# Kernel optimization log

Measured on AMD Instinct MI355X. Metric: run time of the kernel, lower is better.

Reference implementation:

```python
import jax, jax.numpy as jnp
import numpy as np

B, D, H = 524288, 128, 64  # batch, input_dim, hidden_dim; mask_dim = transform_dim = D//2 = 64


def _mlp(x, Wh, bh, Wo, bo):
    """eqx.nn.MLP with depth=3: 3 hidden relu layers then linear out.
    x: [B, in]; Wh: [3, H, in/H]; bh: [3, H]; Wo: [out, H]; bo: [out]."""
    h = x
    for i in range(Wh.shape[0]):  # fixed small layer loop
        h = jax.nn.relu(h @ Wh[i].T + bh[i])
    return h @ Wo.T + bo


def setup_inputs() -> dict:
    key = jax.random.key(0)
    ks = jax.random.split(key, 9)
    m = D // 2
    s = 1.0 / np.sqrt(H)  # lecun-ish init scale
    inp = {"x": jax.random.normal(ks[0], (B, D), dtype=jnp.float32)}
    inp["cond_Wh"] = jax.random.normal(ks[1], (3, H, m), dtype=jnp.float32) * s
    inp["cond_bh"] = jnp.zeros((3, H), dtype=jnp.float32)
    inp["cond_Wo"] = jax.random.normal(ks[2], (D - m, H), dtype=jnp.float32) * s
    inp["cond_bo"] = jnp.zeros((D - m,), dtype=jnp.float32)
    inp["scale_Wh"] = jax.random.normal(ks[3], (3, H, m), dtype=jnp.float32) * s
    inp["scale_bh"] = jnp.zeros((3, H), dtype=jnp.float32)
    inp["scale_Wo"] = jax.random.normal(ks[4], (D - m, H), dtype=jnp.float32) * s
    inp["scale_bo"] = jnp.zeros((D - m,), dtype=jnp.float32)
    return inp


def reference(x, cond_Wh, cond_bh, cond_Wo, cond_bo,
              scale_Wh, scale_bh, scale_Wo, scale_bo):
    m = x.shape[-1] // 2
    # mask = [1]*m + [0]*(D-m) -> mask_idx = [:m], transform_idx = [m:] (static contiguous split)
    x_masked = x[..., :m]
    x_transform = x[..., m:]
    shift = _mlp(x_masked, cond_Wh, cond_bh, cond_Wo, cond_bo)        # [B, D-m]
    log_scale = _mlp(x_masked, scale_Wh, scale_bh, scale_Wo, scale_bo)  # [B, D-m]
    scale = jnp.exp(jnp.clip(log_scale, -5, 3))
    y_transform = x_transform * scale + shift
    y = jnp.concatenate([x_masked, y_transform], axis=-1)  # scatter back (contiguous)
    logdet = jnp.sum(log_scale, axis=-1)  # note: unclipped log_scale, as in original
    return y, logdet
```

## Files before the change

### kernel.cpp

```cpp
#include <hip/hip_runtime.h>
#include <hip/hip_bf16.h>
#include <cstdint>

typedef __attribute__((ext_vector_type(8))) short short8;
typedef __attribute__((ext_vector_type(4))) float f32x4;
typedef __attribute__((ext_vector_type(4))) unsigned int u32x4;

__device__ __forceinline__ uint32_t pk_bf16(float a, float b) {
    uint32_t ua = (uint32_t)__builtin_bit_cast(unsigned short, __float2bfloat16(a));
    uint32_t ub = (uint32_t)__builtin_bit_cast(unsigned short, __float2bfloat16(b));
    return ua | (ub << 16);
}
__device__ __forceinline__ void split_pair(float a, float b, uint32_t& H, uint32_t& L) {
    H = pk_bf16(a, b);
    float fa = __uint_as_float(H << 16);
    float fb = __uint_as_float(H & 0xffff0000u);
    L = pk_bf16(a - fa, b - fb);
}
__device__ __forceinline__ short8 mk8(uint32_t a, uint32_t b, uint32_t c, uint32_t d) {
    u32x4 v; v[0] = a; v[1] = b; v[2] = c; v[3] = d;
    return __builtin_bit_cast(short8, v);
}
__device__ __forceinline__ void cvt_frag(f32x4 A, f32x4 Bv, short8& hi, short8& lo) {
    uint32_t h0, l0, h1, l1, h2, l2, h3, l3;
    split_pair(A[0],  A[1],  h0, l0);
    split_pair(A[2],  A[3],  h1, l1);
    split_pair(Bv[0], Bv[1], h2, l2);
    split_pair(Bv[2], Bv[3], h3, l3);
    hi = mk8(h0, h1, h2, h3);
    lo = mk8(l0, l1, l2, l3);
}

__global__ void prep_weights(const float* __restrict__ cWh, const float* __restrict__ cWo,
                             const float* __restrict__ sWh, const float* __restrict__ sWo,
                             unsigned short* __restrict__ wf) {
    int t = blockIdx.x * 256 + threadIdx.x;
    int e    = t & 7;
    int mt   = (t >> 3) & 3;
    int lane = (t >> 5) & 63;
    int kp   = (t >> 11) & 1;
    int L    = (t >> 12) & 7;
    const float* src = (L < 3)  ? cWh + L * 4096
                     : (L == 3) ? cWo
                     : (L < 7)  ? sWh + (L - 4) * 4096
                     :            sWo;
    int m = mt * 16 + (lane & 15);
    int k = (2 * kp + (e >> 2)) * 16 + 4 * (lane >> 4) + (e & 3);
    float w = src[m * 64 + k];
    uint32_t H, Lo;
    split_pair(w, w, H, Lo);
    int off = lane * 32 + mt * 8 + e;
    int fi = (L * 2 + kp) * 2;
    wf[fi * 2048 + off]        = (unsigned short)H;
    wf[(fi + 1) * 2048 + off]  = (unsigned short)Lo;
}

__device__ __forceinline__ void run_layer(const unsigned short* __restrict__ wf, int Lid,
                                          const float* __restrict__ bias, int lane, int g4,
                                          const short8 Bh[2][4], const short8 Bl[2][4],
                                          f32x4 acc[4][4]) {
#pragma unroll
    for (int mt = 0; mt < 4; ++mt) {
        f32x4 bb = *(const f32x4*)(bias + mt * 16 + g4);
#pragma unroll
        for (int nt = 0; nt < 4; ++nt) acc[mt][nt] = bb;
    }
#pragma unroll
    for (int kp = 0; kp < 2; ++kp) {
        short8 Ah[4], Al[4];
        const unsigned short* p = wf + (Lid * 2 + kp) * 4096 + lane * 32;
#pragma unroll
        for (int mt = 0; mt < 4; ++mt) {
            Ah[mt] = *(const short8*)(p + mt * 8);
            Al[mt] = *(const short8*)(p + 2048 + mt * 8);
        }
#pragma unroll
        for (int nt = 0; nt < 4; ++nt)
#pragma unroll
            for (int mt = 0; mt < 4; ++mt) {
                acc[mt][nt] = __builtin_amdgcn_mfma_f32_16x16x32_bf16(Ah[mt], Bh[kp][nt], acc[mt][nt], 0, 0, 0);
                acc[mt][nt] = __builtin_amdgcn_mfma_f32_16x16x32_bf16(Al[mt], Bh[kp][nt], acc[mt][nt], 0, 0, 0);
                acc[mt][nt] = __builtin_amdgcn_mfma_f32_16x16x32_bf16(Ah[mt], Bl[kp][nt], acc[mt][nt], 0, 0, 0);
            }
    }
}

template<bool RELU>
__device__ __forceinline__ void acc_to_B(const f32x4 acc[4][4], short8 Bh[2][4], short8 Bl[2][4]) {
#pragma unroll
    for (int kp = 0; kp < 2; ++kp)
#pragma unroll
        for (int nt = 0; nt < 4; ++nt) {
            f32x4 a = acc[2 * kp][nt], b = acc[2 * kp + 1][nt];
            if (RELU) {
#pragma unroll
                for (int i = 0; i < 4; ++i) { a[i] = fmaxf(a[i], 0.f); b[i] = fmaxf(b[i], 0.f); }
            }
            cvt_frag(a, b, Bh[kp][nt], Bl[kp][nt]);
        }
}

__global__ __launch_bounds__(64, 2)
void coupling_main(const float* __restrict__ x,
                   const float* __restrict__ cbh, const float* __restrict__ cbo,
                   const float* __restrict__ sbh, const float* __restrict__ sbo,
                   const unsigned short* __restrict__ wf,
                   float* __restrict__ y, float* __restrict__ logdet) {
    const int lane = threadIdx.x;
    const int c = lane & 15;
    const int g4 = (lane >> 4) * 4;
    const long row0 = (long)blockIdx.x * 64;
    const float* xr = x + (row0 + c) * 128 + g4;
    float* yr = y + (row0 + c) * 128 + g4;

    f32x4 xm[4][4];
#pragma unroll
    for (int nt = 0; nt < 4; ++nt)
#pragma unroll
        for (int kt = 0; kt < 4; ++kt)
            xm[nt][kt] = *(const f32x4*)(xr + nt * 2048 + kt * 16);
#pragma unroll
    for (int nt = 0; nt < 4; ++nt)
#pragma unroll
        for (int kt = 0; kt < 4; ++kt)
            *(f32x4*)(yr + nt * 2048 + kt * 16) = xm[nt][kt];

    short8 B0h[2][4], B0l[2][4];
#pragma unroll
    for (int kp = 0; kp < 2; ++kp)
#pragma unroll
        for (int nt = 0; nt < 4; ++nt)
            cvt_frag(xm[nt][2 * kp], xm[nt][2 * kp + 1], B0h[kp][nt], B0l[kp][nt]);

    f32x4 acc[4][4];
    short8 Bh[2][4], Bl[2][4];

    run_layer(wf, 0, cbh,       lane, g4, B0h, B0l, acc);
    acc_to_B<true>(acc, Bh, Bl);
    run_layer(wf, 1, cbh + 64,  lane, g4, Bh, Bl, acc);
    acc_to_B<true>(acc, Bh, Bl);
    run_layer(wf, 2, cbh + 128, lane, g4, Bh, Bl, acc);
    acc_to_B<true>(acc, Bh, Bl);
    run_layer(wf, 3, cbo,       lane, g4, Bh, Bl, acc);
    f32x4 shift[4][4];
#pragma unroll
    for (int mt = 0; mt < 4; ++mt)
#pragma unroll
        for (int nt = 0; nt < 4; ++nt) shift[mt][nt] = acc[mt][nt];

    run_layer(wf, 4, sbh,       lane, g4, B0h, B0l, acc);
    acc_to_B<true>(acc, Bh, Bl);
    run_layer(wf, 5, sbh + 64,  lane, g4, Bh, Bl, acc);
    acc_to_B<true>(acc, Bh, Bl);
    run_layer(wf, 6, sbh + 128, lane, g4, Bh, Bl, acc);
    acc_to_B<true>(acc, Bh, Bl);
    run_layer(wf, 7, sbo,       lane, g4, Bh, Bl, acc);

    f32x4 xt[4][4];
#pragma unroll
    for (int nt = 0; nt < 4; ++nt)
#pragma unroll
        for (int mt = 0; mt < 4; ++mt)
            xt[nt][mt] = *(const f32x4*)(xr + nt * 2048 + 64 + mt * 16);

    float pld0 = 0.f, pld1 = 0.f, pld2 = 0.f, pld3 = 0.f;
#pragma unroll
    for (int nt = 0; nt < 4; ++nt) {
        float psum = 0.f;
#pragma unroll
        for (int mt = 0; mt < 4; ++mt) {
            f32x4 ls = acc[mt][nt];
            psum += ls[0] + ls[1] + ls[2] + ls[3];
            f32x4 o;
#pragma unroll
            for (int i = 0; i < 4; ++i) {
                float cl = fminf(fmaxf(ls[i], -5.f), 3.f);
                o[i] = xt[nt][mt][i] * __expf(cl) + shift[mt][nt][i];
            }
            *(f32x4*)(yr + nt * 2048 + 64 + mt * 16) = o;
        }
        if (nt == 0) pld0 = psum; else if (nt == 1) pld1 = psum;
        else if (nt == 2) pld2 = psum; else pld3 = psum;
    }
#pragma unroll
    for (int nt = 0; nt < 4; ++nt) {
        float v = (nt == 0) ? pld0 : (nt == 1) ? pld1 : (nt == 2) ? pld2 : pld3;
        v += __shfl_xor(v, 16);
        v += __shfl_xor(v, 32);
        if ((lane >> 4) == 0) logdet[row0 + nt * 16 + c] = v;
    }
}

extern "C" void kernel_launch(void* const* d_in, const int* in_sizes, int n_in,
                              void* d_out, int out_size, void* d_ws, size_t ws_size,
                              hipStream_t stream) {
    const float* x   = (const float*)d_in[0];
    const float* cWh = (const float*)d_in[1];
    const float* cbh = (const float*)d_in[2];
    const float* cWo = (const float*)d_in[3];
    const float* cbo = (const float*)d_in[4];
    const float* sWh = (const float*)d_in[5];
    const float* sbh = (const float*)d_in[6];
    const float* sWo = (const float*)d_in[7];
    const float* sbo = (const float*)d_in[8];

    const int B = in_sizes[0] / 128;

    unsigned short* wf = (unsigned short*)d_ws;

    prep_weights<<<128, 256, 0, stream>>>(cWh, cWo, sWh, sWo, wf);

    float* y = (float*)d_out;
    float* logdet = y + (size_t)B * 128;
    coupling_main<<<B / 64, 64, 0, stream>>>(x, cbh, cbo, sbh, sbo, wf, y, logdet);
}
```

Measured before the change: 174.3 us.

## Halve per-wave row tile, pack shift as bf16, use nontemporal stores

```diff
diff --git a/kernel.cpp b/kernel.cpp
--- a/kernel.cpp
+++ b/kernel.cpp
@@ -21,6 +21,9 @@
     u32x4 v; v[0] = a; v[1] = b; v[2] = c; v[3] = d;
     return __builtin_bit_cast(short8, v);
 }
+__device__ __forceinline__ float bf16lo(uint32_t p) { return __uint_as_float(p << 16); }
+__device__ __forceinline__ float bf16hi(uint32_t p) { return __uint_as_float(p & 0xffff0000u); }
+
 __device__ __forceinline__ void cvt_frag(f32x4 A, f32x4 Bv, short8& hi, short8& lo) {
     uint32_t h0, l0, h1, l1, h2, l2, h3, l3;
     split_pair(A[0],  A[1],  h0, l0);
@@ -57,13 +60,13 @@
 
 __device__ __forceinline__ void run_layer(const unsigned short* __restrict__ wf, int Lid,
                                           const float* __restrict__ bias, int lane, int g4,
-                                          const short8 Bh[2][4], const short8 Bl[2][4],
-                                          f32x4 acc[4][4]) {
+                                          const short8 Bh[2][2], const short8 Bl[2][2],
+                                          f32x4 acc[4][2]) {
 #pragma unroll
     for (int mt = 0; mt < 4; ++mt) {
         f32x4 bb = *(const f32x4*)(bias + mt * 16 + g4);
 #pragma unroll
-        for (int nt = 0; nt < 4; ++nt) acc[mt][nt] = bb;
+        for (int nt = 0; nt < 2; ++nt) acc[mt][nt] = bb;
     }
 #pragma unroll
     for (int kp = 0; kp < 2; ++kp) {
@@ -75,7 +78,7 @@
             Al[mt] = *(const short8*)(p + 2048 + mt * 8);
         }
 #pragma unroll
-        for (int nt = 0; nt < 4; ++nt)
+        for (int nt = 0; nt < 2; ++nt)
 #pragma unroll
             for (int mt = 0; mt < 4; ++mt) {
                 acc[mt][nt] = __builtin_amdgcn_mfma_f32_16x16x32_bf16(Ah[mt], Bh[kp][nt], acc[mt][nt], 0, 0, 0);
@@ -85,106 +88,102 @@
     }
 }
 
-template<bool RELU>
-__device__ __forceinline__ void acc_to_B(const f32x4 acc[4][4], short8 Bh[2][4], short8 Bl[2][4]) {
+__device__ __forceinline__ void acc_to_B_relu(const f32x4 acc[4][2], short8 Bh[2][2], short8 Bl[2][2]) {
 #pragma unroll
     for (int kp = 0; kp < 2; ++kp)
 #pragma unroll
-        for (int nt = 0; nt < 4; ++nt) {
+        for (int nt = 0; nt < 2; ++nt) {
             f32x4 a = acc[2 * kp][nt], b = acc[2 * kp + 1][nt];
-            if (RELU) {
-#pragma unroll
-                for (int i = 0; i < 4; ++i) { a[i] = fmaxf(a[i], 0.f); b[i] = fmaxf(b[i], 0.f); }
-            }
+#pragma unroll
+            for (int i = 0; i < 4; ++i) { a[i] = fmaxf(a[i], 0.f); b[i] = fmaxf(b[i], 0.f); }
             cvt_frag(a, b, Bh[kp][nt], Bl[kp][nt]);
         }
 }
 
-__global__ __launch_bounds__(64, 2)
+__global__ __launch_bounds__(256, 3)
 void coupling_main(const float* __restrict__ x,
                    const float* __restrict__ cbh, const float* __restrict__ cbo,
                    const float* __restrict__ sbh, const float* __restrict__ sbo,
                    const unsigned short* __restrict__ wf,
                    float* __restrict__ y, float* __restrict__ logdet) {
-    const int lane = threadIdx.x;
+    const int lane = threadIdx.x & 63;
+    const int wid = threadIdx.x >> 6;
     const int c = lane & 15;
     const int g4 = (lane >> 4) * 4;
-    const long row0 = (long)blockIdx.x * 64;
+    const long row0 = (long)blockIdx.x * 128 + wid * 32;
     const float* xr = x + (row0 + c) * 128 + g4;
     float* yr = y + (row0 + c) * 128 + g4;
 
-    f32x4 xm[4][4];
-#pragma unroll
-    for (int nt = 0; nt < 4; ++nt)
+    f32x4 xm[2][4];
+#pragma unroll
+    for (int nt = 0; nt < 2; ++nt)
 #pragma unroll
         for (int kt = 0; kt < 4; ++kt)
             xm[nt][kt] = *(const f32x4*)(xr + nt * 2048 + kt * 16);
 #pragma unroll
-    for (int nt = 0; nt < 4; ++nt)
+    for (int nt = 0; nt < 2; ++nt)
 #pragma unroll
         for (int kt = 0; kt < 4; ++kt)
-            *(f32x4*)(yr + nt * 2048 + kt * 16) = xm[nt][kt];
-
-    short8 B0h[2][4], B0l[2][4];
+            __builtin_nontemporal_store(xm[nt][kt], (f32x4*)(yr + nt * 2048 + kt * 16));
+
+    short8 B0h[2][2], B0l[2][2];
 #pragma unroll
     for (int kp = 0; kp < 2; ++kp)
 #pragma unroll
-        for (int nt = 0; nt < 4; ++nt)
+        for (int nt = 0; nt < 2; ++nt)
             cvt_frag(xm[nt][2 * kp], xm[nt][2 * kp + 1], B0h[kp][nt], B0l[kp][nt]);
 
-    f32x4 acc[4][4];
-    short8 Bh[2][4], Bl[2][4];
+    f32x4 acc[4][2];
+    short8 Bh[2][2], Bl[2][2];
 
     run_layer(wf, 0, cbh,       lane, g4, B0h, B0l, acc);
-    acc_to_B<true>(acc, Bh, Bl);
+    acc_to_B_relu(acc, Bh, Bl);
     run_layer(wf, 1, cbh + 64,  lane, g4, Bh, Bl, acc);
-    acc_to_B<true>(acc, Bh, Bl);
+    acc_to_B_relu(acc, Bh, Bl);
     run_layer(wf, 2, cbh + 128, lane, g4, Bh, Bl, acc);
-    acc_to_B<true>(acc, Bh, Bl);
+    acc_to_B_relu(acc, Bh, Bl);
     run_layer(wf, 3, cbo,       lane, g4, Bh, Bl, acc);
-    f32x4 shift[4][4];
+    uint2 shiftp[4][2];
 #pragma unroll
     for (int mt = 0; mt < 4; ++mt)
 #pragma unroll
-        for (int nt = 0; nt < 4; ++nt) shift[mt][nt] = acc[mt][nt];
+        for (int nt = 0; nt < 2; ++nt) {
+            f32x4 v = acc[mt][nt];
+            shiftp[mt][nt].x = pk_bf16(v[0], v[1]);
+            shiftp[mt][nt].y = pk_bf16(v[2], v[3]);
+        }
 
     run_layer(wf, 4, sbh,       lane, g4, B0h, B0l, acc);
-    acc_to_B<true>(acc, Bh, Bl);
+    acc_to_B_relu(acc, Bh, Bl);
     run_layer(wf, 5, sbh + 64,  lane, g4, Bh, Bl, acc);
-    acc_to_B<true>(acc, Bh, Bl);
+    acc_to_B_relu(acc, Bh, Bl);
     run_layer(wf, 6, sbh + 128, lane, g4, Bh, Bl, acc);
-    acc_to_B<true>(acc, Bh, Bl);
+    acc_to_B_relu(acc, Bh, Bl);
     run_layer(wf, 7, sbo,       lane, g4, Bh, Bl, acc);
 
-    f32x4 xt[4][4];
-#pragma unroll
-    for (int nt = 0; nt < 4; ++nt)
-#pragma unroll
-        for (int mt = 0; mt < 4; ++mt)
-            xt[nt][mt] = *(const f32x4*)(xr + nt * 2048 + 64 + mt * 16);
-
-    float pld0 = 0.f, pld1 = 0.f, pld2 = 0.f, pld3 = 0.f;
-#pragma unroll
-    for (int nt = 0; nt < 4; ++nt) {
+    float pld0 = 0.f, pld1 = 0.f;
+#pragma unroll
+    for (int nt = 0; nt < 2; ++nt) {
         float psum = 0.f;
 #pragma unroll
         for (int mt = 0; mt < 4; ++mt) {
             f32x4 ls = acc[mt][nt];
             psum += ls[0] + ls[1] + ls[2] + ls[3];
+            f32x4 xt = *(const f32x4*)(xr + nt * 2048 + 64 + mt * 16);
             f32x4 o;
-#pragma unroll
-            for (int i = 0; i < 4; ++i) {
-                float cl = fminf(fmaxf(ls[i], -5.f), 3.f);
-                o[i] = xt[nt][mt][i] * __expf(cl) + shift[mt][nt][i];
-            }
-            *(f32x4*)(yr + nt * 2048 + 64 + mt * 16) = o;
-        }
-        if (nt == 0) pld0 = psum; else if (nt == 1) pld1 = psum;
-        else if (nt == 2) pld2 = psum; else pld3 = psum;
-    }
-#pragma unroll
-    for (int nt = 0; nt < 4; ++nt) {
-        float v = (nt == 0) ? pld0 : (nt == 1) ? pld1 : (nt == 2) ? pld2 : pld3;
+            float s0 = bf16lo(shiftp[mt][nt].x), s1 = bf16hi(shiftp[mt][nt].x);
+            float s2 = bf16lo(shiftp[mt][nt].y), s3 = bf16hi(shiftp[mt][nt].y);
+            o[0] = xt[0] * __expf(fminf(fmaxf(ls[0], -5.f), 3.f)) + s0;
+            o[1] = xt[1] * __expf(fminf(fmaxf(ls[1], -5.f), 3.f)) + s1;
+            o[2] = xt[2] * __expf(fminf(fmaxf(ls[2], -5.f), 3.f)) + s2;
+            o[3] = xt[3] * __expf(fminf(fmaxf(ls[3], -5.f), 3.f)) + s3;
+            __builtin_nontemporal_store(o, (f32x4*)(yr + nt * 2048 + 64 + mt * 16));
+        }
+        if (nt == 0) pld0 = psum; else pld1 = psum;
+    }
+#pragma unroll
+    for (int nt = 0; nt < 2; ++nt) {
+        float v = (nt == 0) ? pld0 : pld1;
         v += __shfl_xor(v, 16);
         v += __shfl_xor(v, 32);
         if ((lane >> 4) == 0) logdet[row0 + nt * 16 + c] = v;
@@ -212,5 +211,5 @@
 
     float* y = (float*)d_out;
     float* logdet = y + (size_t)B * 128;
-    coupling_main<<<B / 64, 64, 0, stream>>>(x, cbh, cbo, sbh, sbo, wf, y, logdet);
-}
+    coupling_main<<<B / 128, 256, 0, stream>>>(x, cbh, cbo, sbh, sbo, wf, y, logdet);
+}
```

Result: slower. 212.5 us (+21.9%).

## Switch split-bf16 MFMA to fp16 with split weights only, shrinking register state

Applied to the files above, without the earlier changes.

```diff
diff --git a/kernel.cpp b/kernel.cpp
--- a/kernel.cpp
+++ b/kernel.cpp
@@ -1,39 +1,13 @@
 #include <hip/hip_runtime.h>
-#include <hip/hip_bf16.h>
 #include <cstdint>
 
-typedef __attribute__((ext_vector_type(8))) short short8;
+typedef __attribute__((ext_vector_type(8))) _Float16 half8;
+typedef __attribute__((ext_vector_type(4))) _Float16 half4;
 typedef __attribute__((ext_vector_type(4))) float f32x4;
-typedef __attribute__((ext_vector_type(4))) unsigned int u32x4;
-
-__device__ __forceinline__ uint32_t pk_bf16(float a, float b) {
-    uint32_t ua = (uint32_t)__builtin_bit_cast(unsigned short, __float2bfloat16(a));
-    uint32_t ub = (uint32_t)__builtin_bit_cast(unsigned short, __float2bfloat16(b));
-    return ua | (ub << 16);
-}
-__device__ __forceinline__ void split_pair(float a, float b, uint32_t& H, uint32_t& L) {
-    H = pk_bf16(a, b);
-    float fa = __uint_as_float(H << 16);
-    float fb = __uint_as_float(H & 0xffff0000u);
-    L = pk_bf16(a - fa, b - fb);
-}
-__device__ __forceinline__ short8 mk8(uint32_t a, uint32_t b, uint32_t c, uint32_t d) {
-    u32x4 v; v[0] = a; v[1] = b; v[2] = c; v[3] = d;
-    return __builtin_bit_cast(short8, v);
-}
-__device__ __forceinline__ void cvt_frag(f32x4 A, f32x4 Bv, short8& hi, short8& lo) {
-    uint32_t h0, l0, h1, l1, h2, l2, h3, l3;
-    split_pair(A[0],  A[1],  h0, l0);
-    split_pair(A[2],  A[3],  h1, l1);
-    split_pair(Bv[0], Bv[1], h2, l2);
-    split_pair(Bv[2], Bv[3], h3, l3);
-    hi = mk8(h0, h1, h2, h3);
-    lo = mk8(l0, l1, l2, l3);
-}
 
 __global__ void prep_weights(const float* __restrict__ cWh, const float* __restrict__ cWo,
                              const float* __restrict__ sWh, const float* __restrict__ sWo,
-                             unsigned short* __restrict__ wf) {
+                             _Float16* __restrict__ wf) {
     int t = blockIdx.x * 256 + threadIdx.x;
     int e    = t & 7;
     int mt   = (t >> 3) & 3;
@@ -47,18 +21,30 @@
     int m = mt * 16 + (lane & 15);
     int k = (2 * kp + (e >> 2)) * 16 + 4 * (lane >> 4) + (e & 3);
     float w = src[m * 64 + k];
-    uint32_t H, Lo;
-    split_pair(w, w, H, Lo);
+    _Float16 hi = (_Float16)w;
+    _Float16 lo = (_Float16)(w - (float)hi);
     int off = lane * 32 + mt * 8 + e;
     int fi = (L * 2 + kp) * 2;
-    wf[fi * 2048 + off]        = (unsigned short)H;
-    wf[(fi + 1) * 2048 + off]  = (unsigned short)Lo;
+    wf[fi * 2048 + off]       = hi;
+    wf[(fi + 1) * 2048 + off] = lo;
 }
 
-__device__ __forceinline__ void run_layer(const unsigned short* __restrict__ wf, int Lid,
+template<bool RELU>
+__device__ __forceinline__ half8 cvt_frag(f32x4 a, f32x4 b) {
+    half8 r;
+#pragma unroll
+    for (int i = 0; i < 4; ++i) {
+        float va = RELU ? fmaxf(a[i], 0.f) : a[i];
+        float vb = RELU ? fmaxf(b[i], 0.f) : b[i];
+        r[i]     = (_Float16)va;
+        r[i + 4] = (_Float16)vb;
+    }
+    return r;
+}
+
+__device__ __forceinline__ void run_layer(const _Float16* __restrict__ wf, int Lid,
                                           const float* __restrict__ bias, int lane, int g4,
-                                          const short8 Bh[2][4], const short8 Bl[2][4],
-                                          f32x4 acc[4][4]) {
+                                          const half8 B[2][4], f32x4 acc[4][4]) {
 #pragma unroll
     for (int mt = 0; mt < 4; ++mt) {
         f32x4 bb = *(const f32x4*)(bias + mt * 16 + g4);
@@ -67,44 +53,36 @@
     }
 #pragma unroll
     for (int kp = 0; kp < 2; ++kp) {
-        short8 Ah[4], Al[4];
-        const unsigned short* p = wf + (Lid * 2 + kp) * 4096 + lane * 32;
+        half8 Ah[4], Al[4];
+        const _Float16* p = wf + (Lid * 2 + kp) * 4096 + lane * 32;
 #pragma unroll
         for (int mt = 0; mt < 4; ++mt) {
-            Ah[mt] = *(const short8*)(p + mt * 8);
-            Al[mt] = *(const short8*)(p + 2048 + mt * 8);
+            Ah[mt] = *(const half8*)(p + mt * 8);
+            Al[mt] = *(const half8*)(p + 2048 + mt * 8);
         }
 #pragma unroll
         for (int nt = 0; nt < 4; ++nt)
 #pragma unroll
             for (int mt = 0; mt < 4; ++mt) {
-                acc[mt][nt] = __builtin_amdgcn_mfma_f32_16x16x32_bf16(Ah[mt], Bh[kp][nt], acc[mt][nt], 0, 0, 0);
-                acc[mt][nt] = __builtin_amdgcn_mfma_f32_16x16x32_bf16(Al[mt], Bh[kp][nt], acc[mt][nt], 0, 0, 0);
-                acc[mt][nt] = __builtin_amdgcn_mfma_f32_16x16x32_bf16(Ah[mt], Bl[kp][nt], acc[mt][nt], 0, 0, 0);
+                acc[mt][nt] = __builtin_amdgcn_mfma_f32_16x16x32_f16(Ah[mt], B[kp][nt], acc[mt][nt], 0, 0, 0);
+                acc[mt][nt] = __builtin_amdgcn_mfma_f32_16x16x32_f16(Al[mt], B[kp][nt], acc[mt][nt], 0, 0, 0);
             }
     }
 }
 
-template<bool RELU>
-__device__ __forceinline__ void acc_to_B(const f32x4 acc[4][4], short8 Bh[2][4], short8 Bl[2][4]) {
+__device__ __forceinline__ void acc_to_B_relu(const f32x4 acc[4][4], half8 B[2][4]) {
 #pragma unroll
     for (int kp = 0; kp < 2; ++kp)
 #pragma unroll
-        for (int nt = 0; nt < 4; ++nt) {
-            f32x4 a = acc[2 * kp][nt], b = acc[2 * kp + 1][nt];
-            if (RELU) {
-#pragma unroll
-                for (int i = 0; i < 4; ++i) { a[i] = fmaxf(a[i], 0.f); b[i] = fmaxf(b[i], 0.f); }
-            }
-            cvt_frag(a, b, Bh[kp][nt], Bl[kp][nt]);
-        }
+        for (int nt = 0; nt < 4; ++nt)
+            B[kp][nt] = cvt_frag<true>(acc[2 * kp][nt], acc[2 * kp + 1][nt]);
 }
 
 __global__ __launch_bounds__(64, 2)
 void coupling_main(const float* __restrict__ x,
                    const float* __restrict__ cbh, const float* __restrict__ cbo,
                    const float* __restrict__ sbh, const float* __restrict__ sbo,
-                   const unsigned short* __restrict__ wf,
+                   const _Float16* __restrict__ wf,
                    float* __restrict__ y, float* __restrict__ logdet) {
     const int lane = threadIdx.x;
     const int c = lane & 15;
@@ -113,55 +91,49 @@
     const float* xr = x + (row0 + c) * 128 + g4;
     float* yr = y + (row0 + c) * 128 + g4;
 
-    f32x4 xm[4][4];
+    half8 B0[2][4];
 #pragma unroll
-    for (int nt = 0; nt < 4; ++nt)
-#pragma unroll
-        for (int kt = 0; kt < 4; ++kt)
-            xm[nt][kt] = *(const f32x4*)(xr + nt * 2048 + kt * 16);
-#pragma unroll
-    for (int nt = 0; nt < 4; ++nt)
-#pragma unroll
-        for (int kt = 0; kt < 4; ++kt)
-            *(f32x4*)(yr + nt * 2048 + kt * 16) = xm[nt][kt];
-
-    short8 B0h[2][4], B0l[2][4];
-#pragma unroll
-    for (int kp = 0; kp < 2; ++kp)
-#pragma unroll
-        for (int nt = 0; nt < 4; ++nt)
-            cvt_frag(xm[nt][2 * kp], xm[nt][2 * kp + 1], B0h[kp][nt], B0l[kp][nt]);
+    for (int nt = 0; nt < 4; ++nt) {
+        f32x4 v0 = *(const f32x4*)(xr + nt * 2048);
+        f32x4 v1 = *(const f32x4*)(xr + nt * 2048 + 16);
+        f32x4 v2 = *(const f32x4*)(xr + nt * 2048 + 32);
+        f32x4 v3 = *(const f32x4*)(xr + nt * 2048 + 48);
+        __builtin_nontemporal_store(v0, (f32x4*)(yr + nt * 2048));
+        __builtin_nontemporal_store(v1, (f32x4*)(yr + nt * 2048 + 16));
+        __builtin_nontemporal_store(v2, (f32x4*)(yr + nt * 2048 + 32));
+        __builtin_nontemporal_store(v3, (f32x4*)(yr + nt * 2048 + 48));
+        B0[0][nt] = cvt_frag<false>(v0, v1);
+        B0[1][nt] = cvt_frag<false>(v2, v3);
+    }
 
     f32x4 acc[4][4];
-    short8 Bh[2][4], Bl[2][4];
+    half8 B[2][4];
 
-    run_layer(wf, 0, cbh,       lane, g4, B0h, B0l, acc);
-    acc_to_B<true>(acc, Bh, Bl);
-    run_layer(wf, 1, cbh + 64,  lane, g4, Bh, Bl, acc);
-    acc_to_B<true>(acc, Bh, Bl);
-    run_layer(wf, 2, cbh + 128, lane, g4, Bh, Bl, acc);
-    acc_to_B<true>(acc, Bh, Bl);
-    run_layer(wf, 3, cbo,       lane, g4, Bh, Bl, acc);
-    f32x4 shift[4][4];
+    run_layer(wf, 0, cbh,       lane, g4, B0, acc);
+    acc_to_B_relu(acc, B);
+    run_layer(wf, 1, cbh + 64,  lane, g4, B, acc);
+    acc_to_B_relu(acc, B);
+    run_layer(wf, 2, cbh + 128, lane, g4, B, acc);
+    acc_to_B_relu(acc, B);
+    run_layer(wf, 3, cbo,       lane, g4, B, acc);
+    half4 shp[4][4];
 #pragma unroll
     for (int mt = 0; mt < 4; ++mt)
 #pragma unroll
-        for (int nt = 0; nt < 4; ++nt) shift[mt][nt] = acc[mt][nt];
+        for (int nt = 0; nt < 4; ++nt) {
+            half4 s;
+#pragma unroll
+            for (int i = 0; i < 4; ++i) s[i] = (_Float16)acc[mt][nt][i];
+            shp[mt][nt] = s;
+        }
 
-    run_layer(wf, 4, sbh,       lane, g4, B0h, B0l, acc);
-    acc_to_B<true>(acc, Bh, Bl);
-    run_layer(wf, 5, sbh + 64,  lane, g4, Bh, Bl, acc);
-    acc_to_B<true>(acc, Bh, Bl);
-    run_layer(wf, 6, sbh + 128, lane, g4, Bh, Bl, acc);
-    acc_to_B<true>(acc, Bh, Bl);
-    run_layer(wf, 7, sbo,       lane, g4, Bh, Bl, acc);
-
-    f32x4 xt[4][4];
-#pragma unroll
-    for (int nt = 0; nt < 4; ++nt)
-#pragma unroll
-        for (int mt = 0; mt < 4; ++mt)
-            xt[nt][mt] = *(const f32x4*)(xr + nt * 2048 + 64 + mt * 16);
+    run_layer(wf, 4, sbh,       lane, g4, B0, acc);
+    acc_to_B_relu(acc, B);
+    run_layer(wf, 5, sbh + 64,  lane, g4, B, acc);
+    acc_to_B_relu(acc, B);
+    run_layer(wf, 6, sbh + 128, lane, g4, B, acc);
+    acc_to_B_relu(acc, B);
+    run_layer(wf, 7, sbo,       lane, g4, B, acc);
 
     float pld0 = 0.f, pld1 = 0.f, pld2 = 0.f, pld3 = 0.f;
 #pragma unroll
@@ -171,13 +143,15 @@
         for (int mt = 0; mt < 4; ++mt) {
             f32x4 ls = acc[mt][nt];
             psum += ls[0] + ls[1] + ls[2] + ls[3];
+            f32x4 xt = *(const f32x4*)(xr + nt * 2048 + 64 + mt * 16);
+            half4 sp = shp[mt][nt];
             f32x4 o;
 #pragma unroll
             for (int i = 0; i < 4; ++i) {
                 float cl = fminf(fmaxf(ls[i], -5.f), 3.f);
-                o[i] = xt[nt][mt][i] * __expf(cl) + shift[mt][nt][i];
+                o[i] = xt[i] * __expf(cl) + (float)sp[i];
             }
-            *(f32x4*)(yr + nt * 2048 + 64 + mt * 16) = o;
+            __builtin_nontemporal_store(o, (f32x4*)(yr + nt * 2048 + 64 + mt * 16));
         }
         if (nt == 0) pld0 = psum; else if (nt == 1) pld1 = psum;
         else if (nt == 2) pld2 = psum; else pld3 = psum;
@@ -206,7 +180,7 @@
 
     const int B = in_sizes[0] / 128;
 
-    unsigned short* wf = (unsigned short*)d_ws;
+    _Float16* wf = (_Float16*)d_ws;
 
     prep_weights<<<128, 256, 0, stream>>>(cWh, cWo, sWh, sWo, wf);
 
```

Result: no change. 173.7 us (-0.4%).
